# Optimization experiments

Measured on AMD Instinct MI355X. Metric: run time of the kernel, lower is better.

## Reference

```python
import jax, jax.numpy as jnp
import numpy as np

B, S = 16, 1                 # decode phase: one new token per sequence
NUM_HEADS, HEAD_DIM = 16, 64
HIDDEN = NUM_HEADS * HEAD_DIM
BLOCK_SIZE = 16
MAX_CTX = 4096               # padded context length (max over sequences)
BLOCKS_PER_SEQ = MAX_CTX // BLOCK_SIZE
MAX_BLOCKS = B * BLOCKS_PER_SEQ


def setup_inputs() -> dict:
    key = jax.random.key(0)
    ks = jax.random.split(key, 8)
    hidden_states = jax.random.normal(ks[0], (B, S, HIDDEN), jnp.float32)
    key_cache = jax.random.normal(ks[1], (MAX_BLOCKS, BLOCK_SIZE, NUM_HEADS, HEAD_DIM), jnp.float32)
    value_cache = jax.random.normal(ks[2], (MAX_BLOCKS, BLOCK_SIZE, NUM_HEADS, HEAD_DIM), jnp.float32)
    # each sequence owns a disjoint set of physical blocks (order = allocation order)
    block_table = jnp.arange(B * BLOCKS_PER_SEQ, dtype=jnp.int32).reshape(B, BLOCKS_PER_SEQ)
    positions = jax.random.randint(ks[3], (B,), 0, MAX_CTX, dtype=jnp.int32)
    wscale = 1.0 / np.sqrt(HIDDEN).astype(np.float32)
    Wq = jax.random.normal(ks[4], (HIDDEN, HIDDEN), jnp.float32) * wscale
    Wk = jax.random.normal(ks[5], (HIDDEN, HIDDEN), jnp.float32) * wscale
    Wv = jax.random.normal(ks[6], (HIDDEN, HIDDEN), jnp.float32) * wscale
    Wo = jax.random.normal(ks[7], (HIDDEN, HIDDEN), jnp.float32) * wscale
    return {
        "hidden_states": hidden_states,
        "key_cache": key_cache,
        "value_cache": value_cache,
        "block_table": block_table,
        "positions": positions,
        "Wq": Wq, "Wk": Wk, "Wv": Wv, "Wo": Wo,
    }


def reference(hidden_states, key_cache, value_cache, block_table, positions, Wq, Wk, Wv, Wo):
    scale = HEAD_DIM ** -0.5
    # projections (torch nn.Linear: x @ W.T)
    q = (hidden_states @ Wq.T).reshape(B, S, NUM_HEADS, HEAD_DIM)
    k_new = (hidden_states @ Wk.T).reshape(B, S, NUM_HEADS, HEAD_DIM)
    v_new = (hidden_states @ Wv.T).reshape(B, S, NUM_HEADS, HEAD_DIM)

    # store_kv: scatter the new token's K/V into the paged cache
    bidx = jnp.arange(B)
    blk = block_table[bidx, positions // BLOCK_SIZE]   # [B]
    slot = positions % BLOCK_SIZE                       # [B]
    key_cache = key_cache.at[blk, slot].set(k_new[:, 0])
    value_cache = value_cache.at[blk, slot].set(v_new[:, 0])

    # get_kv: gather the full (padded) context through the block table
    tok = jnp.arange(MAX_CTX)
    gb = block_table[:, tok // BLOCK_SIZE]              # [B, T] physical block per token
    gs = (tok % BLOCK_SIZE)[None, :]                    # [1, T] slot within block
    K = key_cache[gb, gs]                               # [B, T, H, D]
    V = value_cache[gb, gs]                             # [B, T, H, D]

    # attention with causal/length mask: token t visible iff t <= pos
    scores = jnp.einsum('bqhd,bkhd->bhqk', q, K) * scale   # [B, H, 1, T]
    mask = tok[None, :] <= positions[:, None]               # [B, T]
    scores = jnp.where(mask[:, None, None, :], scores, -jnp.inf)
    attn = jax.nn.softmax(scores, axis=-1)
    out = jnp.einsum('bhqk,bkhd->bqhd', attn, V).reshape(B, S, HIDDEN)
    return out @ Wo.T
```

## Files before the change

### kernel.cpp

```cpp
#include <hip/hip_runtime.h>
#include <math.h>

#define BATCH 16
#define NUM_HEADS 16
#define HEAD_DIM 64
#define HIDDEN 1024
#define BLOCK_SIZE 16
#define MAX_CTX 4096
#define BLOCKS_PER_SEQ 256
#define SPLITS 8
#define CHUNKS 4
#define CHUNK_F4 64

#define Q_OFF   0
#define K_OFF   16384
#define V_OFF   32768
#define AO_OFF  49152
#define PML_OFF 65536
#define PO_OFF  69632
#define PART_OFF 200704

#define LOG2E 1.4426950408889634f

__global__ void proj_partial(const float* __restrict__ X,
                             const float* __restrict__ W0,
                             const float* __restrict__ W1,
                             const float* __restrict__ W2,
                             float* __restrict__ part, int NR) {
    const int tid = threadIdx.x;
    const int b = tid & 15;
    const int r = tid >> 4;
    const int row = blockIdx.x * 16 + r;
    const int c = blockIdx.y;
    const int m = row >> 10;
    const int row_in = row & 1023;
    const float* W = (m == 0) ? W0 : (m == 1) ? W1 : W2;

    const float4* wrow = (const float4*)(W + (size_t)row_in * HIDDEN) + c * CHUNK_F4;
    const float4* xrow = (const float4*)(X + (size_t)b * HIDDEN) + c * CHUNK_F4;
    float acc = 0.f;
#pragma unroll 16
    for (int i = 0; i < CHUNK_F4; ++i) {
        float4 w4 = wrow[i];
        float4 x4 = xrow[i];
        acc += w4.x * x4.x + w4.y * x4.y + w4.z * x4.z + w4.w * x4.w;
    }
    part[((size_t)c * NR + row) * 16 + b] = acc;
}

__global__ void proj_combine(const float* __restrict__ part,
                             float* __restrict__ out0,
                             float* __restrict__ out1,
                             float* __restrict__ out2, int NR) {
    const int idx = blockIdx.x * 256 + threadIdx.x;
    const int row = idx >> 4;
    const int b = idx & 15;
    float s = 0.f;
#pragma unroll
    for (int c = 0; c < CHUNKS; ++c) s += part[((size_t)c * NR + row) * 16 + b];
    const int m = row >> 10;
    const int row_in = row & 1023;
    float* out = (m == 0) ? out0 : (m == 1) ? out1 : out2;
    out[(size_t)b * HIDDEN + row_in] = s;
}

#define LOAD_KV(IT, K0, K1, K2, K3, V0, V1, V2, V3)                              \
    do {                                                                          \
        const int blk_ = bt_lds[(IT) * 4 + w];                                    \
        const size_t base_ = ((size_t)blk_ * BLOCK_SIZE + g) * 1024 + hoff;       \
        const float* kp_ = key_cache + base_;                                     \
        const float* vp_ = value_cache + base_;                                   \
        K0 = *(const float4*)(kp_);                                               \
        K1 = *(const float4*)(kp_ + 4096);                                        \
        K2 = *(const float4*)(kp_ + 8192);                                        \
        K3 = *(const float4*)(kp_ + 12288);                                       \
        V0 = *(const float4*)(vp_);                                               \
        V1 = *(const float4*)(vp_ + 4096);                                        \
        V2 = *(const float4*)(vp_ + 8192);                                        \
        V3 = *(const float4*)(vp_ + 12288);                                       \
    } while (0)

#define COMPUTE(IT, K0, K1, K2, K3, V0, V1, V2, V3)                               \
    do {                                                                          \
        float d0_ = K0.x * q4.x + K0.y * q4.y + K0.z * q4.z + K0.w * q4.w;        \
        float d1_ = K1.x * q4.x + K1.y * q4.y + K1.z * q4.z + K1.w * q4.w;        \
        float d2_ = K2.x * q4.x + K2.y * q4.y + K2.z * q4.z + K2.w * q4.w;        \
        float d3_ = K3.x * q4.x + K3.y * q4.y + K3.z * q4.z + K3.w * q4.w;        \
        d0_ += __shfl_xor(d0_, 1); d1_ += __shfl_xor(d1_, 1);                     \
        d2_ += __shfl_xor(d2_, 1); d3_ += __shfl_xor(d3_, 1);                     \
        d0_ += __shfl_xor(d0_, 2); d1_ += __shfl_xor(d1_, 2);                     \
        d2_ += __shfl_xor(d2_, 2); d3_ += __shfl_xor(d3_, 2);                     \
        d0_ += __shfl_xor(d0_, 4); d1_ += __shfl_xor(d1_, 4);                     \
        d2_ += __shfl_xor(d2_, 4); d3_ += __shfl_xor(d3_, 4);                     \
        d0_ += __shfl_xor(d0_, 8); d1_ += __shfl_xor(d1_, 8);                     \
        d2_ += __shfl_xor(d2_, 8); d3_ += __shfl_xor(d3_, 8);                     \
        const int tb_ = t0 + (IT) * 64 + w * 16 + g;                              \
        if (tb_ + 0  >= t1) d0_ = -INFINITY;                                      \
        if (tb_ + 4  >= t1) d1_ = -INFINITY;                                      \
        if (tb_ + 8  >= t1) d2_ = -INFINITY;                                      \
        if (tb_ + 12 >= t1) d3_ = -INFINITY;                                      \
        const float mx_ = fmaxf(fmaxf(d0_, d1_), fmaxf(d2_, d3_));                \
        const float m_new_ = fmaxf(m, mx_);                                       \
        const float corr_ = exp2f(m - m_new_);                                    \
        const float p0_ = exp2f(d0_ - m_new_);                                    \
        const float p1_ = exp2f(d1_ - m_new_);                                    \
        const float p2_ = exp2f(d2_ - m_new_);                                    \
        const float p3_ = exp2f(d3_ - m_new_);                                    \
        l = l * corr_ + ((p0_ + p1_) + (p2_ + p3_));                              \
        o4.x = o4.x * corr_ + p0_ * V0.x + p1_ * V1.x + p2_ * V2.x + p3_ * V3.x;  \
        o4.y = o4.y * corr_ + p0_ * V0.y + p1_ * V1.y + p2_ * V2.y + p3_ * V3.y;  \
        o4.z = o4.z * corr_ + p0_ * V0.z + p1_ * V1.z + p2_ * V2.z + p3_ * V3.z;  \
        o4.w = o4.w * corr_ + p0_ * V0.w + p1_ * V1.w + p2_ * V2.w + p3_ * V3.w;  \
        m = m_new_;                                                               \
    } while (0)

__global__ void attn_partial(const float* __restrict__ q_ws,
                             const float* __restrict__ key_cache,
                             const float* __restrict__ value_cache,
                             const int* __restrict__ block_table,
                             const int* __restrict__ positions,
                             float* __restrict__ part_ml,
                             float* __restrict__ part_o) {
    const int s = blockIdx.x;
    const int h = blockIdx.y;
    const int b = blockIdx.z;
    const int tid = threadIdx.x;
    const int lane = tid & 63;
    const int w = tid >> 6;
    const int g = lane >> 4;
    const int sub = lane & 15;
    const int gid = w * 4 + g;

    __shared__ int bt_lds[32];
    __shared__ float gm[16];
    __shared__ float gl[16];
    __shared__ float go[16][64];

    const int pos = positions[b];
    const int chunk = ((pos + SPLITS * 64 - 1) / (SPLITS * 64)) * 64;
    const int t0 = s * chunk;
    const int t1 = min(t0 + chunk, pos);
    const int nvalid = t1 - t0;
    const int niter = (nvalid + 63) >> 6;

    float4 q4 = ((const float4*)(q_ws + (size_t)b * HIDDEN + h * HEAD_DIM))[sub];

    if (tid < 32) {
        bt_lds[tid] = block_table[b * BLOCKS_PER_SEQ + (t0 >> 4) + tid];
    }
    __syncthreads();

    const float qs = 0.125f * LOG2E;
    q4.x *= qs; q4.y *= qs; q4.z *= qs; q4.w *= qs;
    const int hoff = h * HEAD_DIM + sub * 4;

    float m = -1e30f;
    float l = 0.f;
    float4 o4 = {0.f, 0.f, 0.f, 0.f};

    float4 kA0, kA1, kA2, kA3, vA0, vA1, vA2, vA3;
    float4 kB0, kB1, kB2, kB3, vB0, vB1, vB2, vB3;

    if (niter > 0) {
        LOAD_KV(0, kA0, kA1, kA2, kA3, vA0, vA1, vA2, vA3);
        int it = 0;
        while (true) {
            if (it + 1 < niter) LOAD_KV(it + 1, kB0, kB1, kB2, kB3, vB0, vB1, vB2, vB3);
            COMPUTE(it, kA0, kA1, kA2, kA3, vA0, vA1, vA2, vA3);
            ++it;
            if (it >= niter) break;
            if (it + 1 < niter) LOAD_KV(it + 1, kA0, kA1, kA2, kA3, vA0, vA1, vA2, vA3);
            COMPUTE(it, kB0, kB1, kB2, kB3, vB0, vB1, vB2, vB3);
            ++it;
            if (it >= niter) break;
        }
    }

    go[gid][sub * 4 + 0] = o4.x;
    go[gid][sub * 4 + 1] = o4.y;
    go[gid][sub * 4 + 2] = o4.z;
    go[gid][sub * 4 + 3] = o4.w;
    if (sub == 0) { gm[gid] = m; gl[gid] = l; }
    __syncthreads();

    if (tid < 64) {
        const int d = tid;
        float M = -1e30f;
#pragma unroll
        for (int gi = 0; gi < 16; ++gi) M = fmaxf(M, gm[gi]);
        float L = 0.f, O = 0.f;
#pragma unroll
        for (int gi = 0; gi < 16; ++gi) {
            const float sc = exp2f(gm[gi] - M);
            L += gl[gi] * sc;
            O += go[gi][d] * sc;
        }
        const int pidx = (b * NUM_HEADS + h) * SPLITS + s;
        part_o[(size_t)pidx * 64 + d] = O;
        if (d == 0) {
            part_ml[pidx * 2 + 0] = M;
            part_ml[pidx * 2 + 1] = L;
        }
    }
}

__global__ void attn_reduce(const float* __restrict__ q_ws,
                            const float* __restrict__ k_ws,
                            const float* __restrict__ v_ws,
                            const float* __restrict__ part_ml,
                            const float* __restrict__ part_o,
                            float* __restrict__ attn_out) {
    const int bh = blockIdx.x;
    const int b = bh >> 4;
    const int h = bh & 15;
    const int d = threadIdx.x;

    const size_t vecoff = (size_t)b * HIDDEN + h * HEAD_DIM + d;
    const float qd = q_ws[vecoff];
    const float kd = k_ws[vecoff];
    float pr = qd * kd;
    pr += __shfl_xor(pr, 1);
    pr += __shfl_xor(pr, 2);
    pr += __shfl_xor(pr, 4);
    pr += __shfl_xor(pr, 8);
    pr += __shfl_xor(pr, 16);
    pr += __shfl_xor(pr, 32);
    const float s_new = pr * (0.125f * LOG2E);

    float M = s_new;
#pragma unroll
    for (int sp = 0; sp < SPLITS; ++sp)
        M = fmaxf(M, part_ml[(bh * SPLITS + sp) * 2]);

    float L = exp2f(s_new - M);
    float O = L * v_ws[vecoff];
#pragma unroll
    for (int sp = 0; sp < SPLITS; ++sp) {
        const float mg = part_ml[(bh * SPLITS + sp) * 2 + 0];
        const float lg = part_ml[(bh * SPLITS + sp) * 2 + 1];
        const float sc = exp2f(mg - M);
        L += lg * sc;
        O += part_o[(size_t)(bh * SPLITS + sp) * 64 + d] * sc;
    }
    attn_out[vecoff] = O / L;
}

extern "C" void kernel_launch(void* const* d_in, const int* in_sizes, int n_in,
                              void* d_out, int out_size, void* d_ws, size_t ws_size,
                              hipStream_t stream) {
    const float* hidden      = (const float*)d_in[0];
    const float* key_cache   = (const float*)d_in[1];
    const float* value_cache = (const float*)d_in[2];
    const int*   block_table = (const int*)d_in[3];
    const int*   positions   = (const int*)d_in[4];
    const float* Wq          = (const float*)d_in[5];
    const float* Wk          = (const float*)d_in[6];
    const float* Wv          = (const float*)d_in[7];
    const float* Wo          = (const float*)d_in[8];
    float* out = (float*)d_out;

    float* ws = (float*)d_ws;
    float* q_ws  = ws + Q_OFF;
    float* k_ws  = ws + K_OFF;
    float* v_ws  = ws + V_OFF;
    float* ao_ws = ws + AO_OFF;
    float* pml   = ws + PML_OFF;
    float* po    = ws + PO_OFF;
    float* part  = ws + PART_OFF;

    proj_partial<<<dim3(192, CHUNKS), 256, 0, stream>>>(hidden, Wq, Wk, Wv, part, 3072);
    proj_combine<<<192, 256, 0, stream>>>(part, q_ws, k_ws, v_ws, 3072);

    attn_partial<<<dim3(SPLITS, NUM_HEADS, BATCH), 256, 0, stream>>>(
        q_ws, key_cache, value_cache, block_table, positions, pml, po);

    attn_reduce<<<BATCH * NUM_HEADS, 64, 0, stream>>>(q_ws, k_ws, v_ws, pml, po, ao_ws);

    proj_partial<<<dim3(64, CHUNKS), 256, 0, stream>>>(ao_ws, Wo, Wo, Wo, part, 1024);
    proj_combine<<<64, 256, 0, stream>>>(part, out, out, out, 1024);
}
```

Before: 94.28 us.

## Fuse QKV split-K combine into attention consumers and double attention splits

Removes the proj_combine launch for the Q/K/V projection. The partial-sum layout becomes chunk-innermost, so attn_partial and attn_reduce each sum the four chunk partials with a single float4 load when they read q, k and v. SPLITS goes from 8 to 16, which roughly halves each split's context chunk, shrinks the block-table LDS buffer to 16, and puts more workgroups on the cache gather. The cost is that every attention split block recomputes the q reduction, and the final reduce has twice as many partials to merge.

```diff
diff --git a/kernel.cpp b/kernel.cpp
--- a/kernel.cpp
+++ b/kernel.cpp
@@ -8,17 +8,14 @@
 #define BLOCK_SIZE 16
 #define MAX_CTX 4096
 #define BLOCKS_PER_SEQ 256
-#define SPLITS 8
+#define SPLITS 16
 #define CHUNKS 4
 #define CHUNK_F4 64
 
-#define Q_OFF   0
-#define K_OFF   16384
-#define V_OFF   32768
-#define AO_OFF  49152
-#define PML_OFF 65536
-#define PO_OFF  69632
-#define PART_OFF 200704
+#define AO_OFF   0
+#define PML_OFF  16384
+#define PO_OFF   24576
+#define PART_OFF 286720
 
 #define LOG2E 1.4426950408889634f
 
@@ -26,7 +23,7 @@
                              const float* __restrict__ W0,
                              const float* __restrict__ W1,
                              const float* __restrict__ W2,
-                             float* __restrict__ part, int NR) {
+                             float* __restrict__ part) {
     const int tid = threadIdx.x;
     const int b = tid & 15;
     const int r = tid >> 4;
@@ -45,23 +42,16 @@
         float4 x4 = xrow[i];
         acc += w4.x * x4.x + w4.y * x4.y + w4.z * x4.z + w4.w * x4.w;
     }
-    part[((size_t)c * NR + row) * 16 + b] = acc;
+    part[((size_t)row * 16 + b) * CHUNKS + c] = acc;
 }
 
 __global__ void proj_combine(const float* __restrict__ part,
-                             float* __restrict__ out0,
-                             float* __restrict__ out1,
-                             float* __restrict__ out2, int NR) {
+                             float* __restrict__ out) {
     const int idx = blockIdx.x * 256 + threadIdx.x;
     const int row = idx >> 4;
     const int b = idx & 15;
-    float s = 0.f;
-#pragma unroll
-    for (int c = 0; c < CHUNKS; ++c) s += part[((size_t)c * NR + row) * 16 + b];
-    const int m = row >> 10;
-    const int row_in = row & 1023;
-    float* out = (m == 0) ? out0 : (m == 1) ? out1 : out2;
-    out[(size_t)b * HIDDEN + row_in] = s;
+    const float4 p = ((const float4*)part)[idx];
+    out[(size_t)b * HIDDEN + row] = p.x + p.y + p.z + p.w;
 }
 
 #define LOAD_KV(IT, K0, K1, K2, K3, V0, V1, V2, V3)                              \
@@ -114,7 +104,7 @@
         m = m_new_;                                                               \
     } while (0)
 
-__global__ void attn_partial(const float* __restrict__ q_ws,
+__global__ void attn_partial(const float* __restrict__ part,
                              const float* __restrict__ key_cache,
                              const float* __restrict__ value_cache,
                              const int* __restrict__ block_table,
@@ -131,7 +121,7 @@
     const int sub = lane & 15;
     const int gid = w * 4 + g;
 
-    __shared__ int bt_lds[32];
+    __shared__ int bt_lds[16];
     __shared__ float gm[16];
     __shared__ float gl[16];
     __shared__ float go[16][64];
@@ -143,15 +133,23 @@
     const int nvalid = t1 - t0;
     const int niter = (nvalid + 63) >> 6;
 
-    float4 q4 = ((const float4*)(q_ws + (size_t)b * HIDDEN + h * HEAD_DIM))[sub];
-
-    if (tid < 32) {
+    const int hbase = h * HEAD_DIM + sub * 4;
+    const float4 pq0 = ((const float4*)part)[(hbase + 0) * 16 + b];
+    const float4 pq1 = ((const float4*)part)[(hbase + 1) * 16 + b];
+    const float4 pq2 = ((const float4*)part)[(hbase + 2) * 16 + b];
+    const float4 pq3 = ((const float4*)part)[(hbase + 3) * 16 + b];
+
+    if (tid < 16) {
         bt_lds[tid] = block_table[b * BLOCKS_PER_SEQ + (t0 >> 4) + tid];
     }
     __syncthreads();
 
     const float qs = 0.125f * LOG2E;
-    q4.x *= qs; q4.y *= qs; q4.z *= qs; q4.w *= qs;
+    float4 q4;
+    q4.x = (pq0.x + pq0.y + pq0.z + pq0.w) * qs;
+    q4.y = (pq1.x + pq1.y + pq1.z + pq1.w) * qs;
+    q4.z = (pq2.x + pq2.y + pq2.z + pq2.w) * qs;
+    q4.w = (pq3.x + pq3.y + pq3.z + pq3.w) * qs;
     const int hoff = h * HEAD_DIM + sub * 4;
 
     float m = -1e30f;
@@ -204,9 +202,7 @@
     }
 }
 
-__global__ void attn_reduce(const float* __restrict__ q_ws,
-                            const float* __restrict__ k_ws,
-                            const float* __restrict__ v_ws,
+__global__ void attn_reduce(const float* __restrict__ part,
                             const float* __restrict__ part_ml,
                             const float* __restrict__ part_o,
                             float* __restrict__ attn_out) {
@@ -215,9 +211,14 @@
     const int h = bh & 15;
     const int d = threadIdx.x;
 
-    const size_t vecoff = (size_t)b * HIDDEN + h * HEAD_DIM + d;
-    const float qd = q_ws[vecoff];
-    const float kd = k_ws[vecoff];
+    const int row = h * HEAD_DIM + d;
+    const float4 pq = ((const float4*)part)[(0    + row) * 16 + b];
+    const float4 pk = ((const float4*)part)[(1024 + row) * 16 + b];
+    const float4 pv = ((const float4*)part)[(2048 + row) * 16 + b];
+    const float qd = pq.x + pq.y + pq.z + pq.w;
+    const float kd = pk.x + pk.y + pk.z + pk.w;
+    const float vd = pv.x + pv.y + pv.z + pv.w;
+
     float pr = qd * kd;
     pr += __shfl_xor(pr, 1);
     pr += __shfl_xor(pr, 2);
@@ -233,7 +234,7 @@
         M = fmaxf(M, part_ml[(bh * SPLITS + sp) * 2]);
 
     float L = exp2f(s_new - M);
-    float O = L * v_ws[vecoff];
+    float O = L * vd;
 #pragma unroll
     for (int sp = 0; sp < SPLITS; ++sp) {
         const float mg = part_ml[(bh * SPLITS + sp) * 2 + 0];
@@ -242,7 +243,7 @@
         L += lg * sc;
         O += part_o[(size_t)(bh * SPLITS + sp) * 64 + d] * sc;
     }
-    attn_out[vecoff] = O / L;
+    attn_out[(size_t)b * HIDDEN + h * HEAD_DIM + d] = O / L;
 }
 
 extern "C" void kernel_launch(void* const* d_in, const int* in_sizes, int n_in,
@@ -260,22 +261,18 @@
     float* out = (float*)d_out;
 
     float* ws = (float*)d_ws;
-    float* q_ws  = ws + Q_OFF;
-    float* k_ws  = ws + K_OFF;
-    float* v_ws  = ws + V_OFF;
     float* ao_ws = ws + AO_OFF;
     float* pml   = ws + PML_OFF;
     float* po    = ws + PO_OFF;
     float* part  = ws + PART_OFF;
 
-    proj_partial<<<dim3(192, CHUNKS), 256, 0, stream>>>(hidden, Wq, Wk, Wv, part, 3072);
-    proj_combine<<<192, 256, 0, stream>>>(part, q_ws, k_ws, v_ws, 3072);
+    proj_partial<<<dim3(192, CHUNKS), 256, 0, stream>>>(hidden, Wq, Wk, Wv, part);
 
     attn_partial<<<dim3(SPLITS, NUM_HEADS, BATCH), 256, 0, stream>>>(
-        q_ws, key_cache, value_cache, block_table, positions, pml, po);
-
-    attn_reduce<<<BATCH * NUM_HEADS, 64, 0, stream>>>(q_ws, k_ws, v_ws, pml, po, ao_ws);
-
-    proj_partial<<<dim3(64, CHUNKS), 256, 0, stream>>>(ao_ws, Wo, Wo, Wo, part, 1024);
-    proj_combine<<<64, 256, 0, stream>>>(part, out, out, out, 1024);
-}
+        part, key_cache, value_cache, block_table, positions, pml, po);
+
+    attn_reduce<<<BATCH * NUM_HEADS, 64, 0, stream>>>(part, pml, po, ao_ws);
+
+    proj_partial<<<dim3(64, CHUNKS), 256, 0, stream>>>(ao_ws, Wo, Wo, Wo, part);
+    proj_combine<<<64, 256, 0, stream>>>(part, out);
+}
```

Result: no change. 96.03 us (+1.9%).
